# Optimization experiments

Measured on AMD Instinct MI355X. Metric: run time of the kernel, lower is better.

Reference implementation:

```python
import jax, jax.numpy as jnp
import numpy as np


def _ramp_filter(H):
    # skimage-style Fourier ramp filter: 2*|f| with f = fftfreq(H)
    f = np.fft.fftfreq(H)
    return (2.0 * np.abs(f)).astype(np.float32)


def setup_inputs() -> dict:
    key = jax.random.key(0)
    N, H_in, W_in, D_out = 8, 768, 360, 512
    radon_image = jax.random.normal(key, (N, 1, H_in, W_in), dtype=jnp.float32)
    hG = jnp.asarray(_ramp_filter(H_in)).reshape(1, 1, H_in, 1)
    return {"radon_image": radon_image, "hG": hG, "D_out": D_out}


def reference(radon_image, hG, D_out):
    N, _, H, W = radon_image.shape
    D = D_out
    # --- Fourier-domain ramp filtering (2D FFT, multiply by real filter along detector axis, real ifft) ---
    X = jnp.fft.fft2(radon_image[:, 0])                     # [N, H, W] complex
    h = hG[0, 0, :, 0]                                      # [H]
    filt = jnp.real(jnp.fft.ifft2(X * h[None, :, None])).astype(radon_image.dtype)  # [N, H, W]

    # --- backprojection grids (matches np.mgrid / tG construction) ---
    Xg, Yg = jnp.meshgrid(jnp.arange(D), jnp.arange(D), indexing="ij")
    xpr = (Xg - D // 2).astype(jnp.float32)
    ypr = (Yg - D // 2).astype(jnp.float32)
    th = (jnp.pi / 180.0) * jnp.linspace(0.0, 180.0, W, endpoint=False)  # [W]
    txs = -1.0 + jnp.arange(W, dtype=jnp.float32) * (2.0 / (W - 1))     # [W]

    hH = H // 2
    sy = (H - 1) / 2.0   # align_corners=True y scale
    sx = (W - 1) / 2.0   # align_corners=True x scale

    def body(recon, angle):
        th_i, tx_i = angle
        t = ypr * jnp.cos(th_i) - xpr * jnp.sin(th_i)       # [D, D]
        py = (t / hH + 1.0) * sy                            # pixel y coords [D, D]
        px = (tx_i + 1.0) * sx                              # scalar pixel x coord
        x0 = jnp.floor(px).astype(jnp.int32)
        wx = px - x0
        y0 = jnp.floor(py).astype(jnp.int32)
        wy = py - y0

        def samp_col(xi):
            vx = ((xi >= 0) & (xi < W)).astype(filt.dtype)
            col = filt[:, :, jnp.clip(xi, 0, W - 1)]        # [N, H]

            def samp_y(yi):
                vy = ((yi >= 0) & (yi < H)).astype(filt.dtype)
                return col[:, jnp.clip(yi, 0, H - 1)] * vy  # [N, D, D] zero-padded

            v = samp_y(y0) * (1.0 - wy) + samp_y(y0 + 1) * wy
            return v * vx

        val = samp_col(x0) * (1.0 - wx) + samp_col(x0 + 1) * wx  # [N, D, D]
        return recon + val, None

    recon0 = jnp.zeros((N, D, D), dtype=radon_image.dtype)
    recon, _ = jax.lax.scan(body, recon0, (th, txs))
    return (recon * (jnp.pi / (2.0 * W)))[:, None]          # [N, 1, D, D]
```

## Files before the change

kernel.cpp:

```cpp
#include <hip/hip_runtime.h>
#include <math.h>

#define N_IMG 8
#define H 768
#define W 360
#define D 512
#define SY 383.5f
#define SC 0.00436332312998582394f
#define NC 24
#define IPAD 384
#define KSTEPS 10

typedef __fp16 h2 __attribute__((ext_vector_type(2)));
struct H2X2 { h2 a, b; };
typedef short short8 __attribute__((ext_vector_type(8)));
typedef float f32x4 __attribute__((ext_vector_type(4)));

__device__ inline unsigned bf16pair(float a, float b) {
    unsigned ua = __builtin_bit_cast(unsigned, a);
    unsigned ub = __builtin_bit_cast(unsigned, b);
    ua += 0x7FFFu + ((ua >> 16) & 1u);
    ub += 0x7FFFu + ((ub >> 16) & 1u);
    return (ua >> 16) | (ub & 0xFFFF0000u);
}

__global__ __launch_bounds__(512)
void k_p0(const float* __restrict__ hG, float* __restrict__ g,
          float4* __restrict__ out4) {
    __shared__ float lred[8];
    const int bid = blockIdx.x, tid = threadIdx.x;

    out4[bid * 512 + tid] = make_float4(0.f, 0.f, 0.f, 0.f);
    if (bid < H) {
        int m = bid;
        int p0 = (tid * m) % H;
        float s = hG[tid] * cosf((float)p0 * 0.00818123086872313911f);
        if (tid < 256) {
            int k = tid + 512;
            int p1 = (k * m) % H;
            s += hG[k] * cosf((float)p1 * 0.00818123086872313911f);
        }
#pragma unroll
        for (int off = 32; off > 0; off >>= 1) s += __shfl_down(s, off);
        if ((tid & 63) == 0) lred[tid >> 6] = s;
        __syncthreads();
        if (tid == 0) {
            float t = 0.f;
#pragma unroll
            for (int w2 = 0; w2 < 8; ++w2) t += lred[w2];
            g[m] = t * (1.0f / (float)H);
        }
    }
}

__global__ __launch_bounds__(512)
void k_p1(const float* __restrict__ radon, const float* __restrict__ g,
          uint4* __restrict__ rcC, uint4* __restrict__ Bg) {
    __shared__ float xs2[2][32][65];
    const int bid = blockIdx.x, tid = threadIdx.x;

    if (bid < 576) {
        const int unit = tid >> 8;
        const int sub  = tid & 255;
        const int tv = bid * 2 + unit;
        float (*xs)[65] = xs2[unit];

        const int i0 = (tv % 6) * 64;
        const int c  = (tv / 6) % NC;
        const int n  = tv / 144;

        {
            int mr    = sub >> 3;
            int lane8 = sub & 7;
            int ib = i0 + lane8 * 8;
            const float* src = radon + ((size_t)n * H + 32 * c + mr) * W + ib;
            float4 v0 = make_float4(0.f, 0.f, 0.f, 0.f), v1 = v0;
            if (ib + 7 < W) {
                v0 = *(const float4*)src;
                v1 = *(const float4*)(src + 4);
            }
            *(float4*)&xs[mr][lane8 * 8]     = v0;
            *(float4*)&xs[mr][lane8 * 8 + 4] = v1;
        }
        __syncthreads();

        const int il  = sub >> 2;
        const int oct = sub & 3;
        float v[8];
#pragma unroll
        for (int s = 0; s < 8; ++s) v[s] = xs[oct * 8 + s][il];
        rcC[(((size_t)n * NC + c) * IPAD + i0 + il) * 4 + oct] =
            (uint4){bf16pair(v[0], v[1]), bf16pair(v[2], v[3]),
                    bf16pair(v[4], v[5]), bf16pair(v[6], v[7])};
    } else if (bid < 581) {
        int idx = (bid - 576) * 512 + tid;
        int L  = idx & 63;
        int tj = idx >> 6;
        int nn = (tj & 3) * 16 + (L & 15);
        int kb = (tj >> 2) * 32 + (L >> 4) * 8;
        float bf[8];
#pragma unroll
        for (int s = 0; s < 8; ++s) {
            int d = nn + 128 - (kb + s);
            d += (d < 0) ? H : 0;
            bf[s] = g[d];
        }
        Bg[idx] = (uint4){bf16pair(bf[0], bf[1]), bf16pair(bf[2], bf[3]),
                          bf16pair(bf[4], bf[5]), bf16pair(bf[6], bf[7])};
    }
}

__global__ __launch_bounds__(512)
void k_p2(const uint4* __restrict__ rcC, const uint4* __restrict__ Bg,
          unsigned short* __restrict__ colp) {
    __shared__ _Float16 lx2[2][16][32][4];
    const int bid = blockIdx.x, tid = threadIdx.x;

    const int unit = tid >> 8;
    const int sub  = tid & 255;
    const int u = bid * 2 + unit;
    _Float16 (*lx)[32][4] = lx2[unit];

    const int yt  = u % 24;
    const int it  = (u / 24) % 23;
    const int grp = u / (24 * 23);
    const int i0 = it * 16, y0 = yt * 32;
    const int wv = sub >> 6, L = sub & 63;

    const int c0 = (yt + 20) % NC;
    const uint4* An = rcC + (size_t)(grp * 4 + wv) * NC * IPAD * 4;
    const int arow = i0 + (L & 15);
    const int aoff = L >> 4;

    f32x4 acc0 = (f32x4){0.f, 0.f, 0.f, 0.f};
    f32x4 acc1 = (f32x4){0.f, 0.f, 0.f, 0.f};

    for (int t = 0; t < KSTEPS; ++t) {
        int c = c0 + t;
        c -= (c >= NC) ? NC : 0;
        short8 a = __builtin_bit_cast(short8, An[((size_t)c * IPAD + arow) * 4 + aoff]);
        short8 b0 = __builtin_bit_cast(short8, Bg[(t * 4 + 0) * 64 + L]);
        short8 b1 = __builtin_bit_cast(short8, Bg[(t * 4 + 1) * 64 + L]);
        acc0 = __builtin_amdgcn_mfma_f32_16x16x32_bf16(a, b0, acc0, 0, 0, 0);
        acc1 = __builtin_amdgcn_mfma_f32_16x16x32_bf16(a, b1, acc1, 0, 0, 0);
    }

#pragma unroll
    for (int r = 0; r < 4; ++r) {
        int ilc = (L >> 4) * 4 + r;
        lx[ilc][(L & 15)][wv]      = (_Float16)(acc0[r] * SC);
        lx[ilc][16 + (L & 15)][wv] = (_Float16)(acc1[r] * SC);
    }
    __syncthreads();

    unsigned short* cp = colp + (size_t)grp * W * H * 4;
#pragma unroll
    for (int k2 = 0; k2 < 2; ++k2) {
        int e = sub + k2 * 256;
        int ilc = e >> 5, ylc = e & 31;
        int ig = i0 + ilc;
        if (ig < W) {
            uint2 v = *(const uint2*)&lx[ilc][ylc][0];
            *(uint2*)&cp[((size_t)ig * H + y0 + ylc) * 4] = v;
        }
    }
}

__global__ __launch_bounds__(512, 8)
void k_p3(const unsigned short* __restrict__ colp, float* __restrict__ outb) {
    __shared__ __align__(16) H2X2 colh[2][H];
    __shared__ float2 angs[W / 4];

    const int bid = blockIdx.x;
    const int bz  = bid & 7;
    const int tle = bid >> 3;
    const int g  = bz >> 2;
    const int aq = bz & 3;
    const int a0 = aq * (W / 4);
    const int u0 = (tle >> 3) * 32;
    const int v0 = (tle & 7) * 64;
    const int tid = threadIdx.x;
    const int lane = tid & 63;
    const int tu = tid >> 6;

    const float vf = (float)(v0 + lane - D / 2);
    float uf[4];
#pragma unroll
    for (int r = 0; r < 4; ++r) uf[r] = (float)(u0 + tu + 8 * r - D / 2);

    const h2 hz = {(__fp16)0.f, (__fp16)0.f};
    float acc[4][4];
    h2 haccA[4], haccB[4];
#pragma unroll
    for (int r = 0; r < 4; ++r) {
#pragma unroll
        for (int nn = 0; nn < 4; ++nn) acc[r][nn] = 0.f;
        haccA[r] = hz;
        haccB[r] = hz;
    }

    const uint2* cp = (const uint2*)colp + (size_t)g * W * H;
    const int y1 = tid;
    const int y2 = tid + 512;

    if (tid < W / 4) {
        float th = (float)(a0 + tid) * 0.00872664625997164788f;
        float r = SY / 384.0f;
        angs[tid] = make_float2(cosf(th) * r, -sinf(th) * r);
    }
    {
        const int ab = a0 * H;
        colh[0][y1] = __builtin_bit_cast(H2X2, cp[ab + y1]);
        if (tid < 256) colh[0][y2] = __builtin_bit_cast(H2X2, cp[ab + y2]);
    }
    __syncthreads();

    for (int j = 0; j < W / 4; ++j) {
        int a = a0 + j;
        int an = (j + 1 < W / 4) ? (a + 1) : a;
        const int ab = an * H;
        uint2 d = cp[ab + y1];
        uint2 e = make_uint2(0u, 0u);
        if (tid < 256) e = cp[ab + y2];

        const int cb2 = j & 1;
        float2 AB = angs[j];
        float base = fmaf(vf, AB.x, SY);
#pragma unroll
        for (int r = 0; r < 4; ++r) {
            float py = fmaf(uf[r], AB.y, base);
            float wy = __builtin_amdgcn_fractf(py);
            int iy = (int)py;
            uint2 lo_raw = *(const uint2*)&colh[cb2][iy];
            uint2 hi_raw = *(const uint2*)&colh[cb2][iy + 1];
            H2X2 lo = __builtin_bit_cast(H2X2, lo_raw);
            H2X2 hi = __builtin_bit_cast(H2X2, hi_raw);
            h2 wy2 = __builtin_amdgcn_cvt_pkrtz(wy, wy);
            haccA[r] += lo.a + wy2 * (hi.a - lo.a);
            haccB[r] += lo.b + wy2 * (hi.b - lo.b);
        }

        if ((j & 15) == 15) {
#pragma unroll
            for (int r = 0; r < 4; ++r) {
                acc[r][0] += (float)haccA[r].x;
                acc[r][1] += (float)haccA[r].y;
                acc[r][2] += (float)haccB[r].x;
                acc[r][3] += (float)haccB[r].y;
                haccA[r] = hz;
                haccB[r] = hz;
            }
        }

        colh[cb2 ^ 1][y1] = __builtin_bit_cast(H2X2, d);
        if (tid < 256) colh[cb2 ^ 1][y2] = __builtin_bit_cast(H2X2, e);
        __syncthreads();
    }

#pragma unroll
    for (int r = 0; r < 4; ++r) {
        acc[r][0] += (float)haccA[r].x;
        acc[r][1] += (float)haccA[r].y;
        acc[r][2] += (float)haccB[r].x;
        acc[r][3] += (float)haccB[r].y;
        int u = u0 + tu + 8 * r;
#pragma unroll
        for (int nn = 0; nn < 4; ++nn) {
            size_t idx = ((size_t)(g * 4 + nn) * D + u) * D + v0 + lane;
            atomicAdd(&outb[idx], acc[r][nn]);
        }
    }
}

extern "C" void kernel_launch(void* const* d_in, const int* in_sizes, int n_in,
                              void* d_out, int out_size, void* d_ws, size_t ws_size,
                              hipStream_t stream) {
    const float* radon = (const float*)d_in[0];
    const float* hG    = (const float*)d_in[1];
    float* out = (float*)d_out;

    float* g    = (float*)d_ws;
    uint4* Bg   = (uint4*)((char*)d_ws + 8192);
    unsigned short* colp = (unsigned short*)((char*)d_ws + 65536);
    uint4* rcC  = (uint4*)((char*)d_ws + 4489216);

    k_p0<<<1024, 512, 0, stream>>>(hG, g, (float4*)out);
    k_p1<<<581, 512, 0, stream>>>(radon, g, rcC, Bg);
    k_p2<<<552, 512, 0, stream>>>(rcC, Bg, colp);
    k_p3<<<1024, 512, 0, stream>>>(colp, out);
}
```

Before: 169.8 us.

## Fuse filter-kernel computation, zeroing and transpose into one pre kernel

Merges the filter coefficient kernel and the transpose/pack kernel into a single launch. Only the needed band of 318 spatial filter taps is computed, inside the tail blocks, and the Bg table is shrunk to the columns the GEMM actually reads. The SC scale moves from the GEMM epilogue into Bg. Output zeroing is spread across the remaining blocks. This removes one kernel launch and the redundant 768-entry cosine sum, at the cost of a heavier serial loop in a few tail blocks that may lengthen the critical path.

```diff
diff --git a/kernel.cpp b/kernel.cpp
--- a/kernel.cpp
+++ b/kernel.cpp
@@ -25,45 +25,22 @@
 }
 
 __global__ __launch_bounds__(512)
-void k_p0(const float* __restrict__ hG, float* __restrict__ g,
-          float4* __restrict__ out4) {
-    __shared__ float lred[8];
+void k_pre(const float* __restrict__ radon, const float* __restrict__ hG,
+           uint4* __restrict__ rcC, uint4* __restrict__ Bg,
+           float4* __restrict__ out4) {
+    __shared__ __align__(16) float smem[2 * 32 * 65];
     const int bid = blockIdx.x, tid = threadIdx.x;
 
-    out4[bid * 512 + tid] = make_float4(0.f, 0.f, 0.f, 0.f);
-    if (bid < H) {
-        int m = bid;
-        int p0 = (tid * m) % H;
-        float s = hG[tid] * cosf((float)p0 * 0.00818123086872313911f);
-        if (tid < 256) {
-            int k = tid + 512;
-            int p1 = (k * m) % H;
-            s += hG[k] * cosf((float)p1 * 0.00818123086872313911f);
-        }
-#pragma unroll
-        for (int off = 32; off > 0; off >>= 1) s += __shfl_down(s, off);
-        if ((tid & 63) == 0) lred[tid >> 6] = s;
-        __syncthreads();
-        if (tid == 0) {
-            float t = 0.f;
-#pragma unroll
-            for (int w2 = 0; w2 < 8; ++w2) t += lred[w2];
-            g[m] = t * (1.0f / (float)H);
-        }
-    }
-}
-
-__global__ __launch_bounds__(512)
-void k_p1(const float* __restrict__ radon, const float* __restrict__ g,
-          uint4* __restrict__ rcC, uint4* __restrict__ Bg) {
-    __shared__ float xs2[2][32][65];
-    const int bid = blockIdx.x, tid = threadIdx.x;
+    {
+        int e = (bid * 512 + tid) * 2;
+        if (e < 524288)     out4[e]     = make_float4(0.f, 0.f, 0.f, 0.f);
+        if (e + 1 < 524288) out4[e + 1] = make_float4(0.f, 0.f, 0.f, 0.f);
+    }
 
     if (bid < 576) {
-        const int unit = tid >> 8;
+        float (*xs)[65] = (float(*)[65])(smem + (tid >> 8) * (32 * 65));
         const int sub  = tid & 255;
-        const int tv = bid * 2 + unit;
-        float (*xs)[65] = xs2[unit];
+        const int tv = bid * 2 + (tid >> 8);
 
         const int i0 = (tv % 6) * 64;
         const int c  = (tv / 6) % NC;
@@ -92,27 +69,52 @@
         rcC[(((size_t)n * NC + c) * IPAD + i0 + il) * 4 + oct] =
             (uint4){bf16pair(v[0], v[1]), bf16pair(v[2], v[3]),
                     bf16pair(v[4], v[5]), bf16pair(v[6], v[7])};
-    } else if (bid < 581) {
-        int idx = (bid - 576) * 512 + tid;
-        int L  = idx & 63;
-        int tj = idx >> 6;
-        int nn = (tj & 3) * 16 + (L & 15);
-        int kb = (tj >> 2) * 32 + (L >> 4) * 8;
-        float bf[8];
-#pragma unroll
-        for (int s = 0; s < 8; ++s) {
-            int d = nn + 128 - (kb + s);
-            d += (d < 0) ? H : 0;
-            bf[s] = g[d];
-        }
-        Bg[idx] = (uint4){bf16pair(bf[0], bf[1]), bf16pair(bf[2], bf[3]),
-                          bf16pair(bf[4], bf[5]), bf16pair(bf[6], bf[7])};
+    } else {
+        float* hgs = smem;
+        float* gl  = smem + 768;
+        const int b = bid - 576;
+        const int lo = 1 - 128 * b;
+
+        hgs[tid] = hG[tid];
+        if (tid < 256) hgs[512 + tid] = hG[512 + tid];
+        __syncthreads();
+
+        if (tid < 318) {
+            int l = tid >> 1, h = tid & 1;
+            int d = lo + l;
+            int dm = d + ((d < 0) ? H : 0);
+            float s = 0.f;
+#pragma unroll 4
+            for (int q = 0; q < 384; ++q) {
+                int k = 384 * h + q;
+                int prod = (k * dm) % H;
+                s += hgs[k] * __builtin_amdgcn_cosf((float)prod * (1.0f / 768.0f));
+            }
+            s += __shfl_xor(s, 1);
+            if (h == 0) gl[l] = s * (1.0f / (float)H);
+        }
+        __syncthreads();
+
+        int idx = b * 512 + tid;
+        if (idx < 1280) {
+            int L   = idx & 63;
+            int tj2 = idx >> 6;
+            int t   = tj2 >> 1, j = tj2 & 1;
+            int nn  = 16 * j + (L & 15);
+            int kb  = 32 * t + (L >> 4) * 8;
+            float bf[8];
+#pragma unroll
+            for (int s = 0; s < 8; ++s)
+                bf[s] = SC * gl[nn + 128 - (kb + s) - lo];
+            Bg[idx] = (uint4){bf16pair(bf[0], bf[1]), bf16pair(bf[2], bf[3]),
+                              bf16pair(bf[4], bf[5]), bf16pair(bf[6], bf[7])};
+        }
     }
 }
 
 __global__ __launch_bounds__(512)
-void k_p2(const uint4* __restrict__ rcC, const uint4* __restrict__ Bg,
-          unsigned short* __restrict__ colp) {
+void k_gemm(const uint4* __restrict__ rcC, const uint4* __restrict__ Bg,
+            unsigned short* __restrict__ colp) {
     __shared__ _Float16 lx2[2][16][32][4];
     const int bid = blockIdx.x, tid = threadIdx.x;
 
@@ -139,8 +141,8 @@
         int c = c0 + t;
         c -= (c >= NC) ? NC : 0;
         short8 a = __builtin_bit_cast(short8, An[((size_t)c * IPAD + arow) * 4 + aoff]);
-        short8 b0 = __builtin_bit_cast(short8, Bg[(t * 4 + 0) * 64 + L]);
-        short8 b1 = __builtin_bit_cast(short8, Bg[(t * 4 + 1) * 64 + L]);
+        short8 b0 = __builtin_bit_cast(short8, Bg[(t * 2 + 0) * 64 + L]);
+        short8 b1 = __builtin_bit_cast(short8, Bg[(t * 2 + 1) * 64 + L]);
         acc0 = __builtin_amdgcn_mfma_f32_16x16x32_bf16(a, b0, acc0, 0, 0, 0);
         acc1 = __builtin_amdgcn_mfma_f32_16x16x32_bf16(a, b1, acc1, 0, 0, 0);
     }
@@ -148,8 +150,8 @@
 #pragma unroll
     for (int r = 0; r < 4; ++r) {
         int ilc = (L >> 4) * 4 + r;
-        lx[ilc][(L & 15)][wv]      = (_Float16)(acc0[r] * SC);
-        lx[ilc][16 + (L & 15)][wv] = (_Float16)(acc1[r] * SC);
+        lx[ilc][(L & 15)][wv]      = (_Float16)acc0[r];
+        lx[ilc][16 + (L & 15)][wv] = (_Float16)acc1[r];
     }
     __syncthreads();
 
@@ -167,7 +169,7 @@
 }
 
 __global__ __launch_bounds__(512, 8)
-void k_p3(const unsigned short* __restrict__ colp, float* __restrict__ outb) {
+void k_bp(const unsigned short* __restrict__ colp, float* __restrict__ outb) {
     __shared__ __align__(16) H2X2 colh[2][H];
     __shared__ float2 angs[W / 4];
 
@@ -279,13 +281,11 @@
     const float* hG    = (const float*)d_in[1];
     float* out = (float*)d_out;
 
-    float* g    = (float*)d_ws;
     uint4* Bg   = (uint4*)((char*)d_ws + 8192);
     unsigned short* colp = (unsigned short*)((char*)d_ws + 65536);
     uint4* rcC  = (uint4*)((char*)d_ws + 4489216);
 
-    k_p0<<<1024, 512, 0, stream>>>(hG, g, (float4*)out);
-    k_p1<<<581, 512, 0, stream>>>(radon, g, rcC, Bg);
-    k_p2<<<552, 512, 0, stream>>>(rcC, Bg, colp);
-    k_p3<<<1024, 512, 0, stream>>>(colp, out);
-}
+    k_pre<<<579, 512, 0, stream>>>(radon, hG, rcC, Bg, (float4*)out);
+    k_gemm<<<552, 512, 0, stream>>>(rcC, Bg, colp);
+    k_bp<<<1024, 512, 0, stream>>>(colp, out);
+}
```

New measurement: 179.2 us. +5.6%, slower.
